# Optimization experiments

Hardware: AMD Instinct MI355X
Metric: run time of the kernel (lower is better)

The kernel has to match this reference:

```python
import jax, jax.numpy as jnp
import numpy as np

BEV = 100  # fixed 100x100 BEV grid from __init__


def _bev_grids():
    # x: arange(-25+0.125, 25, 0.5) -> 100 vals; z: arange(0.125, 50, 0.5) -> 100 vals
    x = jnp.arange(-25.0 + 0.125, 25.0, 0.5, dtype=jnp.float32)
    z = jnp.arange(0.125, 50.0, 0.5, dtype=jnp.float32)
    zz, xx = jnp.meshgrid(z, x, indexing='ij')           # [100,100]
    xz = xx / zz                                          # [100,100]
    yz = jnp.stack([-1.0 / zz, 0.5 / zz, 2.0 / zz], 0)    # [3,100,100], planes y=-1,0.5,2
    return xz, yz


def _grid_sample_bilinear(img, grid):
    """torch.nn.functional.grid_sample, mode='bilinear', padding_mode='zeros',
    align_corners=False. img [B,C,H,W], grid [B,Hg,Wg,2] in [-1,1] (u=x, v=y)."""
    B, C, H, W = img.shape
    x = ((grid[..., 0] + 1.0) * W - 1.0) * 0.5            # unnormalized pixel x
    y = ((grid[..., 1] + 1.0) * H - 1.0) * 0.5
    x0f = jnp.floor(x)
    y0f = jnp.floor(y)
    x0 = x0f.astype(jnp.int32)
    y0 = y0f.astype(jnp.int32)
    x1 = x0 + 1
    y1 = y0 + 1
    wx1 = x - x0f
    wx0 = 1.0 - wx1
    wy1 = y - y0f
    wy0 = 1.0 - wy1

    def corner(xi, yi, w):
        valid = ((xi >= 0) & (xi < W) & (yi >= 0) & (yi < H)).astype(img.dtype)
        xi_c = jnp.clip(xi, 0, W - 1)
        yi_c = jnp.clip(yi, 0, H - 1)
        # per-batch gather: [C,H,W] indexed by [Hg,Wg] -> [C,Hg,Wg]
        vals = jax.vmap(lambda im, yy, xx_: im[:, yy, xx_])(img, yi_c, xi_c)
        return vals * (w * valid)[:, None]                 # [B,C,Hg,Wg]

    return (corner(x0, y0, wx0 * wy0) + corner(x1, y0, wx1 * wy0)
            + corner(x0, y1, wx0 * wy1) + corner(x1, y1, wx1 * wy1))


def setup_inputs() -> dict:
    key = jax.random.key(0)
    k1, k2, k3, k4, k5 = jax.random.split(key, 5)
    B, C, H, W = 8, 512, 88, 176
    img_w, img_h = 704, 352
    img_feature = jax.random.normal(k1, (B, C, H, W), dtype=jnp.float32)
    # realistic pinhole intrinsics so many BEV cells project in-bounds
    fx = jax.random.uniform(k2, (B,), minval=450.0, maxval=650.0)
    fy = jax.random.uniform(k3, (B,), minval=450.0, maxval=650.0)
    cx = img_w / 2.0 + jax.random.uniform(k4, (B,), minval=-8.0, maxval=8.0)
    cy = img_h / 2.0 + jax.random.uniform(k5, (B,), minval=-8.0, maxval=8.0)
    intrinsic = (jnp.zeros((B, 3, 3), dtype=jnp.float32)
                 .at[:, 0, 0].set(fx).at[:, 1, 1].set(fy)
                 .at[:, 0, 2].set(cx).at[:, 1, 2].set(cy)
                 .at[:, 2, 2].set(1.0))
    return {"img_feature": img_feature, "intrinsic": intrinsic,
            "img_w": img_w, "img_h": img_h}


def reference(img_feature, intrinsic, img_w, img_h):
    xz, yz = _bev_grids()
    fx = intrinsic[:, 0, 0][:, None, None]
    cx = intrinsic[:, 0, 2][:, None, None]
    fy = intrinsic[:, 1, 1][:, None, None]
    cy = intrinsic[:, 1, 2][:, None, None]
    u = ((fx * xz[None] + cx) / img_w - 0.5) * 2.0        # [B,100,100], shared by all 3 planes
    acc = None
    for k in range(3):                                     # 3 fixed height planes
        v = ((fy * yz[k][None] + cy) / img_h - 0.5) * 2.0
        grid = jnp.stack((u, v), axis=3)                   # [B,100,100,2]
        s = _grid_sample_bilinear(img_feature, grid)       # [B,C,100,100]
        acc = s if acc is None else acc + s
    return acc / 3.0
```

## Files before the change

kernel.cpp:

```cpp
#include <hip/hip_runtime.h>

#define BEVN 100
#define NB 8
#define NC 512
#define FH 88
#define FW 176
#define HWSZ (FH * FW)
#define NQUAD (BEVN * BEVN / 4)

__global__ __launch_bounds__(1024, 8)
void vt_kernel(const float* __restrict__ img,
               const float* __restrict__ intr,
               const int* __restrict__ p_imw,
               const int* __restrict__ p_imh,
               float* __restrict__ out)
{
    __shared__ float  lds[HWSZ];
    __shared__ float4 ytab[BEVN * 3];

    const int bc  = blockIdx.x;
    const int b   = bc >> 9;
    const int tid = (int)threadIdx.x;

    {
        const float4* __restrict__ s4 = (const float4*)(img + (size_t)bc * HWSZ);
        float4* l4 = (float4*)lds;
        #pragma unroll
        for (int t = 0; t < 4; ++t) {
            const int idx = tid + t * 1024;
            if (idx < HWSZ / 4) l4[idx] = s4[idx];
        }
    }

    const float fx  = intr[b * 9 + 0];
    const float cxv = intr[b * 9 + 2];
    const float fy  = intr[b * 9 + 4];
    const float cyv = intr[b * 9 + 5];
    const float wsc = (float)FW / (float)p_imw[0];
    const float hsc = (float)FH / (float)p_imh[0];

    if (tid < BEVN * 3) {
        const int   i  = tid / 3;
        const int   k  = tid - 3 * i;
        const float z  = 0.125f + 0.5f * (float)i;
        const float iz = 1.0f / z;
        const float yk = (k == 0) ? -1.0f : ((k == 1) ? 0.5f : 2.0f);
        const float yp = fmaf(fy * yk * iz + cyv, hsc, -0.5f);
        const float yf = floorf(yp);
        const int   y0 = (int)yf;
        float wy1 = yp - yf;
        float wy0 = 1.0f - wy1;
        wy0 = ((unsigned)y0 < (unsigned)FH) ? wy0 : 0.0f;
        wy1 = ((unsigned)(y0 + 1) < (unsigned)FH) ? wy1 : 0.0f;
        const int yb0 = min(max(y0, 0), FH - 1) * FW;
        const int yb1 = min(max(y0 + 1, 0), FH - 1) * FW;
        float4 e;
        e.x = wy0 * (1.0f / 3.0f);
        e.y = wy1 * (1.0f / 3.0f);
        e.z = __int_as_float(yb0);
        e.w = __int_as_float(yb1);
        ytab[tid] = e;
    }

    __syncthreads();

    const float axs = 0.5f * fx * wsc;
    const float axb = -24.875f * fx * wsc;
    const float bx  = fmaf(cxv, wsc, -0.5f);

    float* __restrict__ op = out + (size_t)bc * (BEVN * BEVN);

    for (int p = tid; p < NQUAD; p += 1024) {
        const int i  = p / 25;
        const int jq = p - 25 * i;
        const float z    = fmaf(0.5f, (float)i, 0.125f);
        const float invz = __builtin_amdgcn_rcpf(z);

        int   xb[4];
        float w0[4], w1[4];
        #pragma unroll
        for (int e = 0; e < 4; ++e) {
            const float aj   = fmaf((float)(4 * jq + e), axs, axb);
            const float xpix = fmaf(aj, invz, bx);
            const float f    = floorf(xpix);
            const int   x0   = (int)f;
            float wx1 = xpix - f;
            float wx0 = 1.0f - wx1;
            wx0 = ((unsigned)x0 < (unsigned)FW) ? wx0 : 0.0f;
            wx1 = ((unsigned)(x0 + 1) < (unsigned)FW) ? wx1 : 0.0f;
            const int xbe = min(max(x0, 0), FW - 2);
            const int d   = x0 - xbe;
            w0[e] = (d == 0) ? wx0 : ((d < 0) ? wx1 : 0.0f);
            w1[e] = (d == 0) ? wx1 : ((d < 0) ? 0.0f : wx0);
            xb[e] = xbe;
        }

        float4 res;
        const float wsum = (w0[0] + w1[0]) + (w0[1] + w1[1])
                         + (w0[2] + w1[2]) + (w0[3] + w1[3]);
        if (wsum == 0.0f) {
            res.x = res.y = res.z = res.w = 0.0f;
        } else {
            float acc[4] = {0.0f, 0.0f, 0.0f, 0.0f};
            #pragma unroll
            for (int k = 0; k < 3; ++k) {
                const float4 e4  = ytab[i * 3 + k];
                const int    yb0 = __float_as_int(e4.z);
                const int    yb1 = __float_as_int(e4.w);
                #pragma unroll
                for (int e = 0; e < 4; ++e) {
                    const float* r0 = lds + (yb0 + xb[e]);
                    const float* r1 = lds + (yb1 + xb[e]);
                    const float v00 = r0[0], v01 = r0[1];
                    const float v10 = r1[0], v11 = r1[1];
                    const float h0 = fmaf(w1[e], v01, w0[e] * v00);
                    const float h1 = fmaf(w1[e], v11, w0[e] * v10);
                    acc[e] = fmaf(e4.x, h0, acc[e]);
                    acc[e] = fmaf(e4.y, h1, acc[e]);
                }
            }
            res.x = acc[0]; res.y = acc[1]; res.z = acc[2]; res.w = acc[3];
        }
        *(float4*)(op + 4 * p) = res;
    }
}

extern "C" void kernel_launch(void* const* d_in, const int* in_sizes, int n_in,
                              void* d_out, int out_size, void* d_ws, size_t ws_size,
                              hipStream_t stream) {
    const float* img  = (const float*)d_in[0];
    const float* intr = (const float*)d_in[1];
    const int*   imw  = (const int*)d_in[2];
    const int*   imh  = (const int*)d_in[3];
    float*       out  = (float*)d_out;

    dim3 grid(NB * NC);
    dim3 block(1024);
    hipLaunchKernelGGL(vt_kernel, grid, block, 0, stream,
                       img, intr, imw, imh, out);
}
```

Before: 92.36 us.

## Pack two channels as bf16 into shared memory per block

Each block now processes two channels. Both feature maps are converted to bf16 and interleaved into one 32-bit word per pixel, so a single LDS read fetches the same pixel for both channels. This halves the block count and spreads the per-pixel coordinate and weight computation over two channels, at the cost of lower input precision. The bf16 rounding may break a tight fp32 tolerance. Output stores narrow from float4 to two float2 writes.

Result: no change. 91.26 us (-1.2%).

```diff
diff --git a/kernel.cpp b/kernel.cpp
--- a/kernel.cpp
+++ b/kernel.cpp
@@ -6,7 +6,15 @@
 #define FH 88
 #define FW 176
 #define HWSZ (FH * FW)
-#define NQUAD (BEVN * BEVN / 4)
+#define NG4  (HWSZ / 4)
+#define NPAIR (BEVN * BEVN / 2)
+
+__device__ __forceinline__ unsigned bf16rne(float f) {
+    const unsigned b = __float_as_uint(f);
+    return (b + 0x7fffu + ((b >> 16) & 1u)) >> 16;
+}
+__device__ __forceinline__ float lo16f(unsigned u) { return __uint_as_float(u << 16); }
+__device__ __forceinline__ float hi16f(unsigned u) { return __uint_as_float(u & 0xffff0000u); }
 
 __global__ __launch_bounds__(1024, 8)
 void vt_kernel(const float* __restrict__ img,
@@ -15,20 +23,28 @@
                const int* __restrict__ p_imh,
                float* __restrict__ out)
 {
-    __shared__ float  lds[HWSZ];
-    __shared__ float4 ytab[BEVN * 3];
+    __shared__ unsigned lds[HWSZ];
+    __shared__ float4   ytab[BEVN * 3];
 
-    const int bc  = blockIdx.x;
-    const int b   = bc >> 9;
+    const int blk = blockIdx.x;
+    const int b   = blk >> 8;
+    const int c0  = (blk & 255) * 2;
+    const int bc0 = b * NC + c0;
     const int tid = (int)threadIdx.x;
 
     {
-        const float4* __restrict__ s4 = (const float4*)(img + (size_t)bc * HWSZ);
-        float4* l4 = (float4*)lds;
-        #pragma unroll
-        for (int t = 0; t < 4; ++t) {
-            const int idx = tid + t * 1024;
-            if (idx < HWSZ / 4) l4[idx] = s4[idx];
+        const float4* __restrict__ s0 = (const float4*)(img + (size_t)bc0 * HWSZ);
+        const float4* __restrict__ s1 = s0 + NG4;
+        uint4* l4 = (uint4*)lds;
+        for (int idx = tid; idx < NG4; idx += 1024) {
+            const float4 a  = s0[idx];
+            const float4 bb = s1[idx];
+            uint4 u;
+            u.x = bf16rne(a.x) | (bf16rne(bb.x) << 16);
+            u.y = bf16rne(a.y) | (bf16rne(bb.y) << 16);
+            u.z = bf16rne(a.z) | (bf16rne(bb.z) << 16);
+            u.w = bf16rne(a.w) | (bf16rne(bb.w) << 16);
+            l4[idx] = u;
         }
     }
 
@@ -68,19 +84,20 @@
     const float axb = -24.875f * fx * wsc;
     const float bx  = fmaf(cxv, wsc, -0.5f);
 
-    float* __restrict__ op = out + (size_t)bc * (BEVN * BEVN);
+    float* __restrict__ op0 = out + (size_t)bc0 * (BEVN * BEVN);
+    float* __restrict__ op1 = op0 + (BEVN * BEVN);
 
-    for (int p = tid; p < NQUAD; p += 1024) {
-        const int i  = p / 25;
-        const int jq = p - 25 * i;
+    for (int p = tid; p < NPAIR; p += 1024) {
+        const int i  = p / 50;
+        const int jp = p - 50 * i;
         const float z    = fmaf(0.5f, (float)i, 0.125f);
         const float invz = __builtin_amdgcn_rcpf(z);
 
-        int   xb[4];
-        float w0[4], w1[4];
+        int   xb[2];
+        float w0[2], w1[2];
         #pragma unroll
-        for (int e = 0; e < 4; ++e) {
-            const float aj   = fmaf((float)(4 * jq + e), axs, axb);
+        for (int e = 0; e < 2; ++e) {
+            const float aj   = fmaf((float)(2 * jp + e), axs, axb);
             const float xpix = fmaf(aj, invz, bx);
             const float f    = floorf(xpix);
             const int   x0   = (int)f;
@@ -95,33 +112,39 @@
             xb[e] = xbe;
         }
 
-        float4 res;
-        const float wsum = (w0[0] + w1[0]) + (w0[1] + w1[1])
-                         + (w0[2] + w1[2]) + (w0[3] + w1[3]);
+        float2 rA, rB;
+        const float wsum = (w0[0] + w1[0]) + (w0[1] + w1[1]);
         if (wsum == 0.0f) {
-            res.x = res.y = res.z = res.w = 0.0f;
+            rA.x = rA.y = rB.x = rB.y = 0.0f;
         } else {
-            float acc[4] = {0.0f, 0.0f, 0.0f, 0.0f};
+            float accA[2] = {0.0f, 0.0f};
+            float accB[2] = {0.0f, 0.0f};
             #pragma unroll
             for (int k = 0; k < 3; ++k) {
                 const float4 e4  = ytab[i * 3 + k];
                 const int    yb0 = __float_as_int(e4.z);
                 const int    yb1 = __float_as_int(e4.w);
                 #pragma unroll
-                for (int e = 0; e < 4; ++e) {
-                    const float* r0 = lds + (yb0 + xb[e]);
-                    const float* r1 = lds + (yb1 + xb[e]);
-                    const float v00 = r0[0], v01 = r0[1];
-                    const float v10 = r1[0], v11 = r1[1];
-                    const float h0 = fmaf(w1[e], v01, w0[e] * v00);
-                    const float h1 = fmaf(w1[e], v11, w0[e] * v10);
-                    acc[e] = fmaf(e4.x, h0, acc[e]);
-                    acc[e] = fmaf(e4.y, h1, acc[e]);
+                for (int e = 0; e < 2; ++e) {
+                    const unsigned* r0 = lds + (yb0 + xb[e]);
+                    const unsigned* r1 = lds + (yb1 + xb[e]);
+                    const unsigned u00 = r0[0], u01 = r0[1];
+                    const unsigned u10 = r1[0], u11 = r1[1];
+                    const float h0a = fmaf(w1[e], lo16f(u01), w0[e] * lo16f(u00));
+                    const float h1a = fmaf(w1[e], lo16f(u11), w0[e] * lo16f(u10));
+                    accA[e] = fmaf(e4.x, h0a, accA[e]);
+                    accA[e] = fmaf(e4.y, h1a, accA[e]);
+                    const float h0b = fmaf(w1[e], hi16f(u01), w0[e] * hi16f(u00));
+                    const float h1b = fmaf(w1[e], hi16f(u11), w0[e] * hi16f(u10));
+                    accB[e] = fmaf(e4.x, h0b, accB[e]);
+                    accB[e] = fmaf(e4.y, h1b, accB[e]);
                 }
             }
-            res.x = acc[0]; res.y = acc[1]; res.z = acc[2]; res.w = acc[3];
+            rA.x = accA[0]; rA.y = accA[1];
+            rB.x = accB[0]; rB.y = accB[1];
         }
-        *(float4*)(op + 4 * p) = res;
+        *(float2*)(op0 + 2 * p) = rA;
+        *(float2*)(op1 + 2 * p) = rB;
     }
 }
 
@@ -134,7 +157,7 @@
     const int*   imh  = (const int*)d_in[3];
     float*       out  = (float*)d_out;
 
-    dim3 grid(NB * NC);
+    dim3 grid(NB * NC / 2);
     dim3 block(1024);
     hipLaunchKernelGGL(vt_kernel, grid, block, 0, stream,
                        img, intr, imw, imh, out);
```

## Gather bilinear samples directly from global memory instead of staging plane in LDS

Applied to the files above, without the earlier changes.

Drops the step that copied each full 88x176 feature plane into shared memory. Bilinear taps are now read straight from global memory, skipping rows whose vertical weights are both zero. Blocks shrink from 1024 to 256 threads, and each thread handles pairs of output cells instead of quads. This avoids loading the whole plane when only a subset of rows is sampled and lowers LDS pressure so more blocks can be resident, but each tap becomes a scattered global/L2 load.

New measurement: 167.9 us. 81.8% more time.

```diff
diff --git a/kernel.cpp b/kernel.cpp
--- a/kernel.cpp
+++ b/kernel.cpp
@@ -6,31 +6,20 @@
 #define FH 88
 #define FW 176
 #define HWSZ (FH * FW)
-#define NQUAD (BEVN * BEVN / 4)
+#define NPAIR (BEVN * BEVN / 2)
 
-__global__ __launch_bounds__(1024, 8)
+__global__ __launch_bounds__(256, 8)
 void vt_kernel(const float* __restrict__ img,
                const float* __restrict__ intr,
                const int* __restrict__ p_imw,
                const int* __restrict__ p_imh,
                float* __restrict__ out)
 {
-    __shared__ float  lds[HWSZ];
     __shared__ float4 ytab[BEVN * 3];
 
     const int bc  = blockIdx.x;
     const int b   = bc >> 9;
     const int tid = (int)threadIdx.x;
-
-    {
-        const float4* __restrict__ s4 = (const float4*)(img + (size_t)bc * HWSZ);
-        float4* l4 = (float4*)lds;
-        #pragma unroll
-        for (int t = 0; t < 4; ++t) {
-            const int idx = tid + t * 1024;
-            if (idx < HWSZ / 4) l4[idx] = s4[idx];
-        }
-    }
 
     const float fx  = intr[b * 9 + 0];
     const float cxv = intr[b * 9 + 2];
@@ -39,9 +28,9 @@
     const float wsc = (float)FW / (float)p_imw[0];
     const float hsc = (float)FH / (float)p_imh[0];
 
-    if (tid < BEVN * 3) {
-        const int   i  = tid / 3;
-        const int   k  = tid - 3 * i;
+    for (int t = tid; t < BEVN * 3; t += 256) {
+        const int   i  = t / 3;
+        const int   k  = t - 3 * i;
         const float z  = 0.125f + 0.5f * (float)i;
         const float iz = 1.0f / z;
         const float yk = (k == 0) ? -1.0f : ((k == 1) ? 0.5f : 2.0f);
@@ -59,28 +48,28 @@
         e.y = wy1 * (1.0f / 3.0f);
         e.z = __int_as_float(yb0);
         e.w = __int_as_float(yb1);
-        ytab[tid] = e;
+        ytab[t] = e;
     }
-
     __syncthreads();
 
     const float axs = 0.5f * fx * wsc;
     const float axb = -24.875f * fx * wsc;
     const float bx  = fmaf(cxv, wsc, -0.5f);
 
+    const float* __restrict__ sl = img + (size_t)bc * HWSZ;
     float* __restrict__ op = out + (size_t)bc * (BEVN * BEVN);
 
-    for (int p = tid; p < NQUAD; p += 1024) {
-        const int i  = p / 25;
-        const int jq = p - 25 * i;
+    for (int p = tid; p < NPAIR; p += 256) {
+        const int i  = p / 50;
+        const int jp = p - 50 * i;
         const float z    = fmaf(0.5f, (float)i, 0.125f);
         const float invz = __builtin_amdgcn_rcpf(z);
 
-        int   xb[4];
-        float w0[4], w1[4];
+        int   xb[2];
+        float w0[2], w1[2];
         #pragma unroll
-        for (int e = 0; e < 4; ++e) {
-            const float aj   = fmaf((float)(4 * jq + e), axs, axb);
+        for (int e = 0; e < 2; ++e) {
+            const float aj   = fmaf((float)(2 * jp + e), axs, axb);
             const float xpix = fmaf(aj, invz, bx);
             const float f    = floorf(xpix);
             const int   x0   = (int)f;
@@ -95,33 +84,43 @@
             xb[e] = xbe;
         }
 
-        float4 res;
-        const float wsum = (w0[0] + w1[0]) + (w0[1] + w1[1])
-                         + (w0[2] + w1[2]) + (w0[3] + w1[3]);
+        float2 res;
+        const float wsum = (w0[0] + w1[0]) + (w0[1] + w1[1]);
         if (wsum == 0.0f) {
-            res.x = res.y = res.z = res.w = 0.0f;
+            res.x = 0.0f; res.y = 0.0f;
         } else {
-            float acc[4] = {0.0f, 0.0f, 0.0f, 0.0f};
+            float acc0 = 0.0f, acc1 = 0.0f;
             #pragma unroll
             for (int k = 0; k < 3; ++k) {
-                const float4 e4  = ytab[i * 3 + k];
-                const int    yb0 = __float_as_int(e4.z);
-                const int    yb1 = __float_as_int(e4.w);
-                #pragma unroll
-                for (int e = 0; e < 4; ++e) {
-                    const float* r0 = lds + (yb0 + xb[e]);
-                    const float* r1 = lds + (yb1 + xb[e]);
-                    const float v00 = r0[0], v01 = r0[1];
-                    const float v10 = r1[0], v11 = r1[1];
-                    const float h0 = fmaf(w1[e], v01, w0[e] * v00);
-                    const float h1 = fmaf(w1[e], v11, w0[e] * v10);
-                    acc[e] = fmaf(e4.x, h0, acc[e]);
-                    acc[e] = fmaf(e4.y, h1, acc[e]);
+                const float4 e4 = ytab[i * 3 + k];
+                if (e4.x != 0.0f || e4.y != 0.0f) {
+                    const int yb0 = __float_as_int(e4.z);
+                    const int yb1 = __float_as_int(e4.w);
+                    {
+                        const float* r0 = sl + (yb0 + xb[0]);
+                        const float* r1 = sl + (yb1 + xb[0]);
+                        const float v00 = r0[0], v01 = r0[1];
+                        const float v10 = r1[0], v11 = r1[1];
+                        const float h0 = fmaf(w1[0], v01, w0[0] * v00);
+                        const float h1 = fmaf(w1[0], v11, w0[0] * v10);
+                        acc0 = fmaf(e4.x, h0, acc0);
+                        acc0 = fmaf(e4.y, h1, acc0);
+                    }
+                    {
+                        const float* r0 = sl + (yb0 + xb[1]);
+                        const float* r1 = sl + (yb1 + xb[1]);
+                        const float v00 = r0[0], v01 = r0[1];
+                        const float v10 = r1[0], v11 = r1[1];
+                        const float h0 = fmaf(w1[1], v01, w0[1] * v00);
+                        const float h1 = fmaf(w1[1], v11, w0[1] * v10);
+                        acc1 = fmaf(e4.x, h0, acc1);
+                        acc1 = fmaf(e4.y, h1, acc1);
+                    }
                 }
             }
-            res.x = acc[0]; res.y = acc[1]; res.z = acc[2]; res.w = acc[3];
+            res.x = acc0; res.y = acc1;
         }
-        *(float4*)(op + 4 * p) = res;
+        *(float2*)(op + 2 * p) = res;
     }
 }
 
@@ -135,7 +134,7 @@
     float*       out  = (float*)d_out;
 
     dim3 grid(NB * NC);
-    dim3 block(1024);
+    dim3 block(256);
     hipLaunchKernelGGL(vt_kernel, grid, block, 0, stream,
                        img, intr, imw, imh, out);
 }
```
